# Performance work log

Measured on AMD Instinct MI355X. Metric: run time of the kernel, lower is better.

Reference implementation:

```python
import jax, jax.numpy as jnp
import numpy as np

DIM = 4096
HEAD_DIM = 128
N_HEADS = DIM // HEAD_DIM
BSZ = 2
SEQLEN = 1024
CACHE_LEN = 1024


def make_rope_cache(seqlen, head_dim, start_pos, base=10000.0):
    # (seqlen, head_dim//2, 2) holding (cos, sin) at absolute positions
    inv_freq = 1.0 / (base ** (jnp.arange(0, head_dim, 2, dtype=jnp.float32) / head_dim))
    pos = jnp.arange(start_pos, start_pos + seqlen, dtype=jnp.float32)
    ang = pos[:, None] * inv_freq[None, :]  # (s, d/2)
    return jnp.stack([jnp.cos(ang), jnp.sin(ang)], axis=-1)


def setup_inputs() -> dict:
    key = jax.random.key(0)
    ks = jax.random.split(key, 8)
    x = jax.random.normal(ks[0], (BSZ, SEQLEN, DIM), dtype=jnp.float32)
    k_cache = jax.random.normal(ks[1], (BSZ, N_HEADS, CACHE_LEN, HEAD_DIM), dtype=jnp.float32)
    v_cache = jax.random.normal(ks[2], (BSZ, N_HEADS, CACHE_LEN, HEAD_DIM), dtype=jnp.float32)
    rope_cache = make_rope_cache(SEQLEN, HEAD_DIM, CACHE_LEN)
    scale = 0.02
    Wq = jax.random.normal(ks[3], (DIM, DIM), dtype=jnp.float32) * scale
    Wk = jax.random.normal(ks[4], (DIM, DIM), dtype=jnp.float32) * scale
    Wv = jax.random.normal(ks[5], (DIM, DIM), dtype=jnp.float32) * scale
    Wo = jax.random.normal(ks[6], (DIM, DIM), dtype=jnp.float32) * scale
    return {"x": x, "k_cache": k_cache, "v_cache": v_cache, "rope_cache": rope_cache,
            "Wq": Wq, "Wk": Wk, "Wv": Wv, "Wo": Wo}


def _proj_heads(x, W):
    # Linear(dim, dim) with torch convention (out, in), then split heads -> (b, h, s, d)
    b, s, _ = x.shape
    y = jnp.einsum('bsi,oi->bso', x, W)
    return y.reshape(b, s, N_HEADS, HEAD_DIM).transpose(0, 2, 1, 3)


def _apply_rope(t, rope):
    # t: (b, h, s, d); rope: (s, d/2, 2) = (cos, sin)
    b, h, s, d = t.shape
    t2 = t.reshape(b, h, s, d // 2, 2)
    cos = rope[..., 0]  # (s, d/2)
    sin = rope[..., 1]
    t0, t1 = t2[..., 0], t2[..., 1]
    r0 = t0 * cos - t1 * sin
    r1 = t0 * sin + t1 * cos
    return jnp.stack([r0, r1], axis=-1).reshape(b, h, s, d)


def reference(x, k_cache, v_cache, rope_cache, Wq, Wk, Wv, Wo):
    b, s, _ = x.shape
    cache_len = k_cache.shape[2]
    xq = _proj_heads(x, Wq)
    xk = _proj_heads(x, Wk)
    xv = _proj_heads(x, Wv)
    xq = _apply_rope(xq, rope_cache)
    xk = _apply_rope(xk, rope_cache)
    xk = jnp.concatenate([k_cache, xk], axis=2)  # (b, h, cache+s, d)
    xv = jnp.concatenate([v_cache, xv], axis=2)
    scale = 1.0 / jnp.sqrt(jnp.asarray(HEAD_DIM, dtype=x.dtype))
    scores = jnp.einsum('bhsd,bhtd->bhst', xq, xk) * scale
    # causal: query at absolute position cache_len+i attends to keys j <= cache_len+i
    q_pos = jnp.arange(s) + cache_len
    k_pos = jnp.arange(cache_len + s)
    mask = k_pos[None, :] <= q_pos[:, None]  # (s, t)
    scores = jnp.where(mask[None, None], scores, jnp.asarray(-1e30, dtype=scores.dtype))
    attn = jax.nn.softmax(scores, axis=-1)
    ctx = jnp.einsum('bhst,bhtd->bhsd', attn, xv)
    ctx = ctx.transpose(0, 2, 1, 3).reshape(b, s, DIM)
    output = jnp.einsum('bsi,oi->bso', ctx, Wo)  # dropout is identity at p=0 / eval
    return (output, xk, xv)
```

## Files before the change

kernel.cpp:

```cpp
#include <hip/hip_runtime.h>
#include <cstdint>
#include <cstddef>

typedef unsigned short u16;
typedef __attribute__((ext_vector_type(8))) short bf16x8;
typedef __attribute__((ext_vector_type(4))) float f32x4;

using gas_ptr = const __attribute__((address_space(1))) void*;
using las_ptr = __attribute__((address_space(3))) void*;

__device__ __forceinline__ u16 f2bf(float f) {
  union { float f; unsigned int u; } v; v.f = f;
  unsigned int u = v.u;
  return (u16)((u + 0x7fffu + ((u >> 16) & 1u)) >> 16);
}

__device__ __forceinline__ float fast_exp2(float x) {
  return __builtin_amdgcn_exp2f(x);
}

__global__ __launch_bounds__(256) void cvt_f32_bf16(const float* __restrict__ src,
                                                    u16* __restrict__ dst, int n) {
  int i = (blockIdx.x * 256 + threadIdx.x) * 4;
  if (i >= n) return;
  float4 v = *(const float4*)(src + i);
  ushort4 o;
  o.x = f2bf(v.x); o.y = f2bf(v.y); o.z = f2bf(v.z); o.w = f2bf(v.w);
  *(ushort4*)(dst + i) = o;
}

__global__ __launch_bounds__(256) void gemm_bt(const u16* __restrict__ A,
                                               const u16* __restrict__ B,
                                               float* __restrict__ C,
                                               int M, int N, int K) {
  __shared__ u16 As[128][32];
  __shared__ u16 Bs[128][32];
  const int m0 = blockIdx.y * 128, n0 = blockIdx.x * 128;
  const int tid = threadIdx.x;
  const int wave = tid >> 6, lane = tid & 63;
  const int wm = (wave & 1) * 64, wn = (wave >> 1) * 64;
  const int srow = lane >> 2, skoff = (lane & 3) * 8;
  const int col = lane & 15, quad = lane >> 4;
  f32x4 acc[4][4] = {};
  for (int k0 = 0; k0 < K; k0 += 32) {
#pragma unroll
    for (int r = 0; r < 2; ++r) {
      const u16* ga = A + (size_t)(m0 + r * 64 + wave * 16 + srow) * K + k0 + skoff;
      const u16* gb = B + (size_t)(n0 + r * 64 + wave * 16 + srow) * K + k0 + skoff;
      __builtin_amdgcn_global_load_lds((gas_ptr)ga, (las_ptr)&As[r * 64 + wave * 16][0], 16, 0, 0);
      __builtin_amdgcn_global_load_lds((gas_ptr)gb, (las_ptr)&Bs[r * 64 + wave * 16][0], 16, 0, 0);
    }
    __syncthreads();
    bf16x8 af[4], bfr[4];
#pragma unroll
    for (int t = 0; t < 4; ++t) {
      af[t]  = *(const bf16x8*)&As[wm + t * 16 + col][quad * 8];
      bfr[t] = *(const bf16x8*)&Bs[wn + t * 16 + col][quad * 8];
    }
#pragma unroll
    for (int mt = 0; mt < 4; ++mt)
#pragma unroll
      for (int nt = 0; nt < 4; ++nt)
        acc[mt][nt] = __builtin_amdgcn_mfma_f32_16x16x32_bf16(af[mt], bfr[nt], acc[mt][nt], 0, 0, 0);
    __syncthreads();
  }
#pragma unroll
  for (int mt = 0; mt < 4; ++mt)
#pragma unroll
    for (int nt = 0; nt < 4; ++nt)
#pragma unroll
      for (int r = 0; r < 4; ++r) {
        const int row  = m0 + wm + mt * 16 + quad * 4 + r;
        const int ccol = n0 + wn + nt * 16 + col;
        C[(size_t)row * N + ccol] = acc[mt][nt][r];
      }
}


#define BAR   __builtin_amdgcn_s_barrier()
#define LGKM0 asm volatile("s_waitcnt lgkmcnt(0)" ::: "memory")
#define VM4   asm volatile("s_waitcnt vmcnt(4)" ::: "memory")
#define VM0   asm volatile("s_waitcnt vmcnt(0)" ::: "memory")

#define STAGE(AB, G, H, T)                                                             \
  do {                                                                                 \
    _Pragma("unroll")                                                                  \
    for (int q = 0; q < 2; ++q) {                                                      \
      const int rl = wave * 16 + q * 8 + (lane >> 3);                                  \
      const int sc = (lane & 7) ^ (rl & 7);                                            \
      __builtin_amdgcn_global_load_lds(                                                \
          (gas_ptr)((G) + (size_t)((H) * 128 + rl) * K + (T) * 64 + sc * 8),           \
          (las_ptr)&sm[(T) & 1][AB][H][wave * 16 + q * 8][0], 16, 0, 0);               \
    }                                                                                  \
  } while (0)

#define LDA(DST, BUF, MH)                                                              \
  do {                                                                                 \
    _Pragma("unroll")                                                                  \
    for (int mi = 0; mi < 4; ++mi)                                                     \
      _Pragma("unroll")                                                                \
      for (int kc = 0; kc < 2; ++kc)                                                   \
        DST[mi][kc] = *(const bf16x8*)&sm[BUF][0][wm][(MH) * 64 + mi * 16 + col]       \
                                         [((kc * 4 + quad) ^ (col & 7)) << 3];         \
  } while (0)

#define LDB(BUF, NH)                                                                   \
  do {                                                                                 \
    _Pragma("unroll")                                                                  \
    for (int ni = 0; ni < 2; ++ni)                                                     \
      _Pragma("unroll")                                                                \
      for (int kc = 0; kc < 2; ++kc)                                                   \
        bb[ni][kc] = *(const bf16x8*)&sm[BUF][1][wn >> 1]                              \
                                        [(wn & 1) * 64 + (NH) * 32 + ni * 16 + col]    \
                                        [((kc * 4 + quad) ^ (col & 7)) << 3];          \
  } while (0)

#define MFMA16(MH, NH, AR)                                                             \
  do {                                                                                 \
    __builtin_amdgcn_s_setprio(1);                                                     \
    _Pragma("unroll")                                                                  \
    for (int mi = 0; mi < 4; ++mi)                                                     \
      _Pragma("unroll")                                                                \
      for (int ni = 0; ni < 2; ++ni)                                                   \
        _Pragma("unroll")                                                              \
        for (int kc = 0; kc < 2; ++kc)                                                 \
          acc[(MH) * 4 + mi][(NH) * 2 + ni] = __builtin_amdgcn_mfma_f32_16x16x32_bf16( \
              AR[mi][kc], bb[ni][kc], acc[(MH) * 4 + mi][(NH) * 2 + ni], 0, 0, 0);     \
    __builtin_amdgcn_s_setprio(0);                                                     \
  } while (0)

__global__ __launch_bounds__(512, 2) void gemm_bt_256(const u16* __restrict__ A,
                                                      const u16* __restrict__ B,
                                                      float* __restrict__ C,
                                                      int M, int N, int K) {
  __shared__ u16 sm[2][2][2][128][64];
  const int tid  = threadIdx.x;
  const int wave = tid >> 6, lane = tid & 63;
  const int wm   = wave >> 2, wn = wave & 3;
  const int col  = lane & 15, quad = lane >> 4;

  const int bid = blockIdx.y * gridDim.x + blockIdx.x;
  int m_idx, n_idx;
  if (gridDim.x == 48 && gridDim.y == 8) {
    const int x = bid & 7;
    const int r = bid >> 3;
    m_idx = r & 7;
    n_idx = x * 6 + (r >> 3);
  } else {
    m_idx = bid / gridDim.x;
    n_idx = bid % gridDim.x;
  }
  const int m0 = m_idx * 256;
  const int n0 = n_idx * 256;

  const u16* Ag = A + (size_t)m0 * K;
  const u16* Bg = B + (size_t)n0 * K;

  f32x4 acc[8][4] = {};
  bf16x8 a0[4][2], a1[4][2], bb[2][2];

  STAGE(0, Ag, 0, 0); STAGE(0, Ag, 1, 0);
  STAGE(1, Bg, 0, 0); STAGE(1, Bg, 1, 0);
  STAGE(0, Ag, 0, 1); STAGE(0, Ag, 1, 1);
  VM4;
  BAR;

  const int NIT = K >> 7;
  for (int i = 0; i < NIT - 1; ++i) {
    const int t0 = i * 2;
    LDA(a0, 0, 0); LDB(0, 0); STAGE(1, Bg, 0, t0 + 1);
    LGKM0; MFMA16(0, 0, a0); BAR;
    LDA(a1, 0, 1); STAGE(1, Bg, 1, t0 + 1);
    LGKM0; MFMA16(1, 0, a1); BAR;
    LDB(0, 1); STAGE(0, Ag, 0, t0 + 2);
    LGKM0; MFMA16(1, 1, a1); BAR;
    STAGE(0, Ag, 1, t0 + 2);
    LGKM0; MFMA16(0, 1, a0); VM4; BAR;
    LDA(a0, 1, 0); LDB(1, 0); STAGE(1, Bg, 0, t0 + 2);
    LGKM0; MFMA16(0, 0, a0); BAR;
    LDA(a1, 1, 1); STAGE(1, Bg, 1, t0 + 2);
    LGKM0; MFMA16(1, 0, a1); BAR;
    LDB(1, 1); STAGE(0, Ag, 0, t0 + 3);
    LGKM0; MFMA16(1, 1, a1); BAR;
    STAGE(0, Ag, 1, t0 + 3);
    LGKM0; MFMA16(0, 1, a0); VM4; BAR;
  }
  {
    const int t0 = 2 * NIT - 2;
    LDA(a0, 0, 0); LDB(0, 0); STAGE(1, Bg, 0, t0 + 1);
    LGKM0; MFMA16(0, 0, a0); BAR;
    LDA(a1, 0, 1); STAGE(1, Bg, 1, t0 + 1);
    LGKM0; MFMA16(1, 0, a1); BAR;
    LDB(0, 1);
    LGKM0; MFMA16(1, 1, a1); BAR;
    LGKM0; MFMA16(0, 1, a0); VM0; BAR;
    LDA(a0, 1, 0); LDB(1, 0);
    LGKM0; MFMA16(0, 0, a0); BAR;
    LDA(a1, 1, 1);
    LGKM0; MFMA16(1, 0, a1); BAR;
    LDB(1, 1);
    LGKM0; MFMA16(1, 1, a1); BAR;
    LGKM0; MFMA16(0, 1, a0);
  }

#pragma unroll
  for (int mi = 0; mi < 8; ++mi)
#pragma unroll
    for (int ni = 0; ni < 4; ++ni)
#pragma unroll
      for (int r = 0; r < 4; ++r) {
        const int row = m0 + wm * 128 + mi * 16 + quad * 4 + r;
        const int cc  = n0 + wn * 64 + ni * 16 + col;
        C[(size_t)row * N + cc] = acc[mi][ni][r];
      }
}

#undef STAGE
#undef LDA
#undef LDB
#undef MFMA16
#undef BAR
#undef LGKM0
#undef VM4
#undef VM0

__global__ __launch_bounds__(256) void rope_q_kernel(const float* __restrict__ qkv,
                                                     const float* __restrict__ rope,
                                                     u16* __restrict__ Qb) {
  const float qs = 0.08838834764831845f * 1.4426950408889634f;
  int idx = blockIdx.x * 256 + threadIdx.x;
  int i = idx & 63, s = (idx >> 6) & 1023, bh = idx >> 16;
  int b = bh >> 5, h = bh & 31;
  const float* p = qkv + (size_t)(b * 1024 + s) * 12288 + h * 128 + 2 * i;
  float t0 = p[0], t1 = p[1];
  float c = rope[(s * 64 + i) * 2], sn = rope[(s * 64 + i) * 2 + 1];
  size_t o = ((size_t)bh * 1024 + s) * 128 + 2 * i;
  Qb[o]     = f2bf((t0 * c - t1 * sn) * qs);
  Qb[o + 1] = f2bf((t0 * sn + t1 * c) * qs);
}

__global__ __launch_bounds__(256) void rope_k_kernel(const float* __restrict__ qkv,
                                                     const float* __restrict__ rope,
                                                     float* __restrict__ xk,
                                                     u16* __restrict__ Kb) {
  int idx = blockIdx.x * 256 + threadIdx.x;
  int i = idx & 63, s = (idx >> 6) & 1023, bh = idx >> 16;
  int b = bh >> 5, h = bh & 31;
  const float* p = qkv + (size_t)(b * 1024 + s) * 12288 + 4096 + h * 128 + 2 * i;
  float t0 = p[0], t1 = p[1];
  float c = rope[(s * 64 + i) * 2], sn = rope[(s * 64 + i) * 2 + 1];
  float r0 = t0 * c - t1 * sn, r1 = t0 * sn + t1 * c;
  size_t o = ((size_t)bh * 2048 + 1024 + s) * 128 + 2 * i;
  xk[o] = r0; xk[o + 1] = r1;
  Kb[o] = f2bf(r0); Kb[o + 1] = f2bf(r1);
}

__global__ __launch_bounds__(256) void copy_v_kernel(const float* __restrict__ qkv,
                                                     float* __restrict__ xv) {
  int idx = blockIdx.x * 256 + threadIdx.x;
  int d = idx & 127, s = (idx >> 7) & 1023, bh = idx >> 17;
  int b = bh >> 5, h = bh & 31;
  xv[((size_t)bh * 2048 + 1024 + s) * 128 + d] =
      qkv[(size_t)(b * 1024 + s) * 12288 + 8192 + h * 128 + d];
}

__global__ __launch_bounds__(256) void cache_copy_k_kernel(const float* __restrict__ src,
                                                           float* __restrict__ dst,
                                                           u16* __restrict__ dstb) {
  int idx = blockIdx.x * 256 + threadIdx.x;
  int d = idx & 127, t = (idx >> 7) & 1023, bh = idx >> 17;
  float v = src[idx];
  size_t o = ((size_t)bh * 2048 + t) * 128 + d;
  dst[o] = v;
  dstb[o] = f2bf(v);
}

__global__ __launch_bounds__(256) void cache_copy_v_kernel(const float* __restrict__ src,
                                                           float* __restrict__ dst) {
  int idx = blockIdx.x * 256 + threadIdx.x;
  int d = idx & 127, t = (idx >> 7) & 1023, bh = idx >> 17;
  dst[((size_t)bh * 2048 + t) * 128 + d] = src[idx];
}

__global__ __launch_bounds__(256) void transpose_v_kernel(const float* __restrict__ src,
                                                          u16* __restrict__ dst) {
  __shared__ float tile[32][33];
  int bh = blockIdx.z;
  int t0 = blockIdx.x * 32, d0 = blockIdx.y * 32;
  int tx = threadIdx.x & 31, ty = threadIdx.x >> 5;
  const float* s = src + ((size_t)bh * 2048 + t0) * 128 + d0;
#pragma unroll
  for (int i = 0; i < 4; ++i)
    tile[ty + i * 8][tx] = s[(ty + i * 8) * 128 + tx];
  __syncthreads();
  u16* dp = dst + ((size_t)bh * 128 + d0) * 2048 + t0;
#pragma unroll
  for (int i = 0; i < 4; ++i)
    dp[(ty + i * 8) * 2048 + tx] = f2bf(tile[tx][ty + i * 8]);
}

__global__ __launch_bounds__(256, 2) void attn_kernel(const u16* __restrict__ Qb,
                                                      const u16* __restrict__ Kb,
                                                      const u16* __restrict__ VT,
                                                      u16* __restrict__ ctx) {
  const int bh = blockIdx.y;
  const int b = bh >> 5, h = bh & 31;
  const int wave = threadIdx.x >> 6, lane = threadIdx.x & 63;
  const int col = lane & 15, quad = lane >> 4;
  const int qblk = blockIdx.x * 128;
  const int qw = qblk + wave * 32;

  __shared__ u16 Ks[64][128];
  __shared__ u16 Vs[128][64];
  __shared__ u16 Plds[4][32][64];

  const u16* Qh = Qb + (size_t)bh * 1024 * 128;
  const u16* Kh = Kb + (size_t)bh * 2048 * 128;
  const u16* Vh = VT + (size_t)bh * 128 * 2048;

  bf16x8 qf[2][4];
#pragma unroll
  for (int mt = 0; mt < 2; ++mt)
#pragma unroll
    for (int kc = 0; kc < 4; ++kc)
      qf[mt][kc] = *(const bf16x8*)&Qh[(size_t)(qw + mt * 16 + col) * 128 + kc * 32 + quad * 8];

  f32x4 o[2][8] = {};
  float m_r[2][4], l_r[2][4];
#pragma unroll
  for (int mt = 0; mt < 2; ++mt)
#pragma unroll
    for (int r = 0; r < 4; ++r) { m_r[mt][r] = -1e30f; l_r[mt][r] = 0.0f; }

  const int t_end = 1024 + qblk + 128;

  for (int t0 = 0; t0 < t_end; t0 += 64) {
#pragma unroll
    for (int j = 0; j < 4; ++j) {
      const int g = j * 4 + wave;
      const int r = g * 4 + (lane >> 4);
      const int cg = (lane & 15) ^ (r & 15);
      __builtin_amdgcn_global_load_lds((gas_ptr)(Kh + (size_t)(t0 + r) * 128 + cg * 8),
                                       (las_ptr)&Ks[g * 4][0], 16, 0, 0);
    }
#pragma unroll
    for (int j = 0; j < 4; ++j) {
      const int g = j * 4 + wave;
      const int r = g * 8 + (lane >> 3);
      const int cg = (lane & 7) ^ (r & 7);
      __builtin_amdgcn_global_load_lds((gas_ptr)(Vh + (size_t)r * 2048 + t0 + cg * 8),
                                       (las_ptr)&Vs[g * 8][0], 16, 0, 0);
    }
    __syncthreads();

    f32x4 s[2][4];
#pragma unroll
    for (int mt = 0; mt < 2; ++mt)
#pragma unroll
      for (int tt = 0; tt < 4; ++tt) s[mt][tt] = (f32x4){0.f, 0.f, 0.f, 0.f};
#pragma unroll
    for (int kc = 0; kc < 4; ++kc) {
      bf16x8 kf[4];
#pragma unroll
      for (int tt = 0; tt < 4; ++tt)
        kf[tt] = *(const bf16x8*)&Ks[tt * 16 + col][(((kc * 4 + quad) ^ col) & 15) * 8];
#pragma unroll
      for (int mt = 0; mt < 2; ++mt)
#pragma unroll
        for (int tt = 0; tt < 4; ++tt)
          s[mt][tt] = __builtin_amdgcn_mfma_f32_16x16x32_bf16(qf[mt][kc], kf[tt], s[mt][tt], 0, 0, 0);
    }

#pragma unroll
    for (int mt = 0; mt < 2; ++mt)
#pragma unroll
      for (int r = 0; r < 4; ++r) {
        const int qabs = 1024 + qw + mt * 16 + quad * 4 + r;
        float v[4];
#pragma unroll
        for (int tt = 0; tt < 4; ++tt) {
          v[tt] = s[mt][tt][r];
          if (t0 + tt * 16 + col > qabs) v[tt] = -1e30f;
        }
        float mx = fmaxf(fmaxf(v[0], v[1]), fmaxf(v[2], v[3]));
        mx = fmaxf(mx, __shfl_xor(mx, 1));
        mx = fmaxf(mx, __shfl_xor(mx, 2));
        mx = fmaxf(mx, __shfl_xor(mx, 4));
        mx = fmaxf(mx, __shfl_xor(mx, 8));
        const float mnew  = fmaxf(m_r[mt][r], mx);
        const float alpha = fast_exp2(m_r[mt][r] - mnew);
        m_r[mt][r] = mnew;
        float sum = 0.f;
#pragma unroll
        for (int tt = 0; tt < 4; ++tt) {
          v[tt] = fast_exp2(v[tt] - mnew);
          sum += v[tt];
        }
        sum += __shfl_xor(sum, 1);
        sum += __shfl_xor(sum, 2);
        sum += __shfl_xor(sum, 4);
        sum += __shfl_xor(sum, 8);
        l_r[mt][r] = l_r[mt][r] * alpha + sum;
#pragma unroll
        for (int dt = 0; dt < 8; ++dt) o[mt][dt][r] *= alpha;
        const int prow = mt * 16 + quad * 4 + r;
#pragma unroll
        for (int tt = 0; tt < 4; ++tt) {
          const int t = tt * 16 + col;
          const int c = (t >> 3) ^ (prow & 7);
          Plds[wave][prow][c * 8 + (t & 7)] = f2bf(v[tt]);
        }
      }
    asm volatile("s_waitcnt lgkmcnt(0)" ::: "memory");

    bf16x8 pf[2][2];
#pragma unroll
    for (int mt = 0; mt < 2; ++mt)
#pragma unroll
      for (int kk = 0; kk < 2; ++kk)
        pf[mt][kk] = *(const bf16x8*)&Plds[wave][mt * 16 + col][(((kk * 4 + quad) ^ (col & 7))) * 8];
#pragma unroll
    for (int kk = 0; kk < 2; ++kk)
#pragma unroll
      for (int dt = 0; dt < 8; ++dt) {
        bf16x8 vf = *(const bf16x8*)&Vs[dt * 16 + col][(((kk * 4 + quad) ^ (col & 7))) * 8];
#pragma unroll
        for (int mt = 0; mt < 2; ++mt)
          o[mt][dt] = __builtin_amdgcn_mfma_f32_16x16x32_bf16(pf[mt][kk], vf, o[mt][dt], 0, 0, 0);
      }
    __syncthreads();
  }

  float inv[2][4];
#pragma unroll
  for (int mt = 0; mt < 2; ++mt)
#pragma unroll
    for (int r = 0; r < 4; ++r) inv[mt][r] = 1.0f / l_r[mt][r];
#pragma unroll
  for (int mt = 0; mt < 2; ++mt)
#pragma unroll
    for (int dt = 0; dt < 8; ++dt)
#pragma unroll
      for (int r = 0; r < 4; ++r) {
        const int q = qw + mt * 16 + quad * 4 + r;
        const int d = dt * 16 + col;
        ctx[(size_t)(b * 1024 + q) * 4096 + h * 128 + d] = f2bf(o[mt][dt][r] * inv[mt][r]);
      }
}

extern "C" void kernel_launch(void* const* d_in, const int* in_sizes, int n_in,
                              void* d_out, int out_size, void* d_ws, size_t ws_size,
                              hipStream_t stream) {
  const float* x    = (const float*)d_in[0];
  const float* kc   = (const float*)d_in[1];
  const float* vc   = (const float*)d_in[2];
  const float* rope = (const float*)d_in[3];
  const float* Wq   = (const float*)d_in[4];
  const float* Wk   = (const float*)d_in[5];
  const float* Wv   = (const float*)d_in[6];
  const float* Wo   = (const float*)d_in[7];

  float* out = (float*)d_out;
  float* xk  = out + 8388608;
  float* xv  = out + 25165824;

  char* ws = (char*)d_ws;
  u16*   Xb   = (u16*)(ws + 0);
  u16*   Wc   = (u16*)(ws + 16777216);
  u16*   KbB  = (u16*)(ws + 16777216);
  u16*   VTb  = (u16*)(ws + 50331648);
  float* QKV  = (float*)(ws + 117440512);
  u16*   Wob  = (u16*)(ws + 117440512);
  u16*   ctxb = (u16*)(ws + 150994944);
  u16*   Qbb  = (u16*)(ws + 218103808);

  cvt_f32_bf16<<<8192, 256, 0, stream>>>(x, Xb, 8388608);
  cvt_f32_bf16<<<16384, 256, 0, stream>>>(Wq, Wc, 16777216);
  cvt_f32_bf16<<<16384, 256, 0, stream>>>(Wk, Wc + 16777216, 16777216);
  cvt_f32_bf16<<<16384, 256, 0, stream>>>(Wv, Wc + 33554432, 16777216);
  gemm_bt_256<<<dim3(48, 8), 512, 0, stream>>>(Xb, Wc, QKV, 2048, 12288, 4096);
  rope_q_kernel<<<16384, 256, 0, stream>>>(QKV, rope, Qbb);
  rope_k_kernel<<<16384, 256, 0, stream>>>(QKV, rope, xk, KbB);
  copy_v_kernel<<<32768, 256, 0, stream>>>(QKV, xv);
  cache_copy_k_kernel<<<32768, 256, 0, stream>>>(kc, xk, KbB);
  cache_copy_v_kernel<<<32768, 256, 0, stream>>>(vc, xv);
  transpose_v_kernel<<<dim3(64, 4, 64), 256, 0, stream>>>(xv, VTb);
  cvt_f32_bf16<<<16384, 256, 0, stream>>>(Wo, Wob, 16777216);
  attn_kernel<<<dim3(8, 64), 256, 0, stream>>>(Qbb, KbB, VTb, ctxb);
  gemm_bt<<<dim3(32, 16), 256, 0, stream>>>(ctxb, Wob, out, 2048, 4096, 4096);
}
```

Baseline: 992.8 us.

## Fuse RoPE, head split and V copy into QKV GEMM epilogue; merge small kernels

The QKV GEMM epilogue now applies RoPE with a lane-shuffle partner exchange. It writes Q as bf16, K as fp32 plus bf16, and V as fp32 straight into the head-major output layouts, so the fp32 QKV intermediate and three follow-up kernels are no longer needed. The three weight-conversion launches are merged into one, and the K and V cache copies are merged into one kernel. This cuts a large fp32 intermediate round trip and several launches. In exchange, the epilogue does scattered writes and rope loads, which may be less coalesced.

New measurement: 984.5 us. Within noise of the previous version (-0.8%).

```diff
diff --git a/kernel.cpp b/kernel.cpp
--- a/kernel.cpp
+++ b/kernel.cpp
@@ -24,6 +24,21 @@
   int i = (blockIdx.x * 256 + threadIdx.x) * 4;
   if (i >= n) return;
   float4 v = *(const float4*)(src + i);
+  ushort4 o;
+  o.x = f2bf(v.x); o.y = f2bf(v.y); o.z = f2bf(v.z); o.w = f2bf(v.w);
+  *(ushort4*)(dst + i) = o;
+}
+
+__global__ __launch_bounds__(256) void cvt3_w(const float* __restrict__ Wq,
+                                              const float* __restrict__ Wk,
+                                              const float* __restrict__ Wv,
+                                              u16* __restrict__ dst) {
+  int i = (blockIdx.x * 256 + threadIdx.x) * 4;
+  const float* src; int off;
+  if (i < 16777216)      { src = Wq; off = i; }
+  else if (i < 33554432) { src = Wk; off = i - 16777216; }
+  else                   { src = Wv; off = i - 33554432; }
+  float4 v = *(const float4*)(src + off);
   ushort4 o;
   o.x = f2bf(v.x); o.y = f2bf(v.y); o.z = f2bf(v.z); o.w = f2bf(v.w);
   *(ushort4*)(dst + i) = o;
@@ -129,10 +144,14 @@
     __builtin_amdgcn_s_setprio(0);                                                     \
   } while (0)
 
-__global__ __launch_bounds__(512, 2) void gemm_bt_256(const u16* __restrict__ A,
-                                                      const u16* __restrict__ B,
-                                                      float* __restrict__ C,
-                                                      int M, int N, int K) {
+__global__ __launch_bounds__(512, 2) void gemm_qkv(const u16* __restrict__ A,
+                                                   const u16* __restrict__ B,
+                                                   const float* __restrict__ rope,
+                                                   u16* __restrict__ Qb,
+                                                   float* __restrict__ xk,
+                                                   u16* __restrict__ Kb,
+                                                   float* __restrict__ xv,
+                                                   int M, int N, int K) {
   __shared__ u16 sm[2][2][2][128][64];
   const int tid  = threadIdx.x;
   const int wave = tid >> 6, lane = tid & 63;
@@ -203,6 +222,9 @@
     LGKM0; MFMA16(0, 1, a0);
   }
 
+  const float qs = 0.08838834764831845f * 1.4426950408889634f;
+  const int kind = n0 >> 12;
+  const int colb = n0 + wn * 64 + (lane & 15);
 #pragma unroll
   for (int mi = 0; mi < 8; ++mi)
 #pragma unroll
@@ -210,8 +232,25 @@
 #pragma unroll
       for (int r = 0; r < 4; ++r) {
         const int row = m0 + wm * 128 + mi * 16 + quad * 4 + r;
-        const int cc  = n0 + wn * 64 + ni * 16 + col;
-        C[(size_t)row * N + cc] = acc[mi][ni][r];
+        const int b_ = row >> 10, s = row & 1023;
+        const int cc = colb + ni * 16;
+        float v = acc[mi][ni][r];
+        if (kind == 2) {
+          const int c2 = cc - 8192;
+          xv[((size_t)(b_ * 32 + (c2 >> 7)) * 2048 + 1024 + s) * 128 + (c2 & 127)] = v;
+        } else {
+          const float partner = __shfl_xor(v, 1);
+          const int c2 = cc & 4095, d = c2 & 127, h = c2 >> 7;
+          const int ri = (s * 64 + (d >> 1)) * 2;
+          const float cz = rope[ri], sn = rope[ri + 1];
+          const float ov = (d & 1) ? (partner * sn + v * cz) : (v * cz - partner * sn);
+          if (kind == 0) {
+            Qb[((size_t)(b_ * 32 + h) * 1024 + s) * 128 + d] = f2bf(ov * qs);
+          } else {
+            const size_t o = ((size_t)(b_ * 32 + h) * 2048 + 1024 + s) * 128 + d;
+            xk[o] = ov; Kb[o] = f2bf(ov);
+          }
+        }
       }
 }
 
@@ -224,62 +263,17 @@
 #undef VM4
 #undef VM0
 
-__global__ __launch_bounds__(256) void rope_q_kernel(const float* __restrict__ qkv,
-                                                     const float* __restrict__ rope,
-                                                     u16* __restrict__ Qb) {
-  const float qs = 0.08838834764831845f * 1.4426950408889634f;
-  int idx = blockIdx.x * 256 + threadIdx.x;
-  int i = idx & 63, s = (idx >> 6) & 1023, bh = idx >> 16;
-  int b = bh >> 5, h = bh & 31;
-  const float* p = qkv + (size_t)(b * 1024 + s) * 12288 + h * 128 + 2 * i;
-  float t0 = p[0], t1 = p[1];
-  float c = rope[(s * 64 + i) * 2], sn = rope[(s * 64 + i) * 2 + 1];
-  size_t o = ((size_t)bh * 1024 + s) * 128 + 2 * i;
-  Qb[o]     = f2bf((t0 * c - t1 * sn) * qs);
-  Qb[o + 1] = f2bf((t0 * sn + t1 * c) * qs);
-}
-
-__global__ __launch_bounds__(256) void rope_k_kernel(const float* __restrict__ qkv,
-                                                     const float* __restrict__ rope,
-                                                     float* __restrict__ xk,
-                                                     u16* __restrict__ Kb) {
-  int idx = blockIdx.x * 256 + threadIdx.x;
-  int i = idx & 63, s = (idx >> 6) & 1023, bh = idx >> 16;
-  int b = bh >> 5, h = bh & 31;
-  const float* p = qkv + (size_t)(b * 1024 + s) * 12288 + 4096 + h * 128 + 2 * i;
-  float t0 = p[0], t1 = p[1];
-  float c = rope[(s * 64 + i) * 2], sn = rope[(s * 64 + i) * 2 + 1];
-  float r0 = t0 * c - t1 * sn, r1 = t0 * sn + t1 * c;
-  size_t o = ((size_t)bh * 2048 + 1024 + s) * 128 + 2 * i;
-  xk[o] = r0; xk[o + 1] = r1;
-  Kb[o] = f2bf(r0); Kb[o + 1] = f2bf(r1);
-}
-
-__global__ __launch_bounds__(256) void copy_v_kernel(const float* __restrict__ qkv,
-                                                     float* __restrict__ xv) {
-  int idx = blockIdx.x * 256 + threadIdx.x;
-  int d = idx & 127, s = (idx >> 7) & 1023, bh = idx >> 17;
-  int b = bh >> 5, h = bh & 31;
-  xv[((size_t)bh * 2048 + 1024 + s) * 128 + d] =
-      qkv[(size_t)(b * 1024 + s) * 12288 + 8192 + h * 128 + d];
-}
-
-__global__ __launch_bounds__(256) void cache_copy_k_kernel(const float* __restrict__ src,
-                                                           float* __restrict__ dst,
-                                                           u16* __restrict__ dstb) {
+__global__ __launch_bounds__(256) void cache_copy_kernel(const float* __restrict__ kc,
+                                                         const float* __restrict__ vc,
+                                                         float* __restrict__ xk,
+                                                         float* __restrict__ xv,
+                                                         u16* __restrict__ Kb) {
   int idx = blockIdx.x * 256 + threadIdx.x;
   int d = idx & 127, t = (idx >> 7) & 1023, bh = idx >> 17;
-  float v = src[idx];
   size_t o = ((size_t)bh * 2048 + t) * 128 + d;
-  dst[o] = v;
-  dstb[o] = f2bf(v);
-}
-
-__global__ __launch_bounds__(256) void cache_copy_v_kernel(const float* __restrict__ src,
-                                                           float* __restrict__ dst) {
-  int idx = blockIdx.x * 256 + threadIdx.x;
-  int d = idx & 127, t = (idx >> 7) & 1023, bh = idx >> 17;
-  dst[((size_t)bh * 2048 + t) * 128 + d] = src[idx];
+  float k = kc[idx], v = vc[idx];
+  xk[o] = k; Kb[o] = f2bf(k);
+  xv[o] = v;
 }
 
 __global__ __launch_bounds__(256) void transpose_v_kernel(const float* __restrict__ src,
@@ -467,23 +461,17 @@
   char* ws = (char*)d_ws;
   u16*   Xb   = (u16*)(ws + 0);
   u16*   Wc   = (u16*)(ws + 16777216);
-  u16*   KbB  = (u16*)(ws + 16777216);
   u16*   VTb  = (u16*)(ws + 50331648);
-  float* QKV  = (float*)(ws + 117440512);
   u16*   Wob  = (u16*)(ws + 117440512);
   u16*   ctxb = (u16*)(ws + 150994944);
+  u16*   KbB  = (u16*)(ws + 184549376);
   u16*   Qbb  = (u16*)(ws + 218103808);
 
   cvt_f32_bf16<<<8192, 256, 0, stream>>>(x, Xb, 8388608);
-  cvt_f32_bf16<<<16384, 256, 0, stream>>>(Wq, Wc, 16777216);
-  cvt_f32_bf16<<<16384, 256, 0, stream>>>(Wk, Wc + 16777216, 16777216);
-  cvt_f32_bf16<<<16384, 256, 0, stream>>>(Wv, Wc + 33554432, 16777216);
-  gemm_bt_256<<<dim3(48, 8), 512, 0, stream>>>(Xb, Wc, QKV, 2048, 12288, 4096);
-  rope_q_kernel<<<16384, 256, 0, stream>>>(QKV, rope, Qbb);
-  rope_k_kernel<<<16384, 256, 0, stream>>>(QKV, rope, xk, KbB);
-  copy_v_kernel<<<32768, 256, 0, stream>>>(QKV, xv);
-  cache_copy_k_kernel<<<32768, 256, 0, stream>>>(kc, xk, KbB);
-  cache_copy_v_kernel<<<32768, 256, 0, stream>>>(vc, xv);
+  cvt3_w<<<49152, 256, 0, stream>>>(Wq, Wk, Wv, Wc);
+  gemm_qkv<<<dim3(48, 8), 512, 0, stream>>>(Xb, Wc, rope, Qbb, xk, KbB, xv,
+                                            2048, 12288, 4096);
+  cache_copy_kernel<<<32768, 256, 0, stream>>>(kc, vc, xk, xv, KbB);
   transpose_v_kernel<<<dim3(64, 4, 64), 256, 0, stream>>>(xv, VTb);
   cvt_f32_bf16<<<16384, 256, 0, stream>>>(Wo, Wob, 16777216);
   attn_kernel<<<dim3(8, 64), 256, 0, stream>>>(Qbb, KbB, VTb, ctxb);
```
